# Performance work log

Measured on AMD Instinct MI355X. Metric: run time of the kernel, lower is better.

The kernel has to match this reference:

```python
import jax, jax.numpy as jnp
import numpy as np

N = 65536        # lattice nodes (256x256 grid)
E_RAND = 1_000_000  # non-self-loop causal edges (~16 per node)
T = 65           # max edge type after add_self_loops (type 1 = self loop)
FIN = 8
FOUT = 8
B = 16           # batch of spin configurations


def setup_inputs() -> dict:
    key = jax.random.key(0)
    k1, k2, k3, k4, k5, k6 = jax.random.split(key, 6)
    x = jax.random.normal(k1, (N, FIN, B), dtype=jnp.float32)
    bound = 1.0 / np.sqrt(FIN)  # matches reset_parameters uniform init
    W = jax.random.uniform(k2, (T, FOUT, FIN), jnp.float32, -bound, bound)
    b = jax.random.uniform(k3, (T, FOUT), jnp.float32, -bound, bound)
    # add_self_loops: identity edges with type 1, other types shifted to 2..T
    loops = jnp.arange(N, dtype=jnp.int32)
    src = jnp.concatenate([loops, jax.random.randint(k4, (E_RAND,), 0, N, dtype=jnp.int32)])
    tgt = jnp.concatenate([loops, jax.random.randint(k5, (E_RAND,), 0, N, dtype=jnp.int32)])
    etype = jnp.concatenate([
        jnp.ones((N,), dtype=jnp.int32),
        jax.random.randint(k6, (E_RAND,), 2, T + 1, dtype=jnp.int32),
    ])
    return {"x": x, "W": W, "b": b, "src": src, "tgt": tgt, "etype": etype}


def reference(x, W, b, src, tgt, etype):
    # Faithful to GraphConvLayer.forward (depth=None): the expanded sparse
    # weight matrix assigns a unique [FOUT,FIN] block W[t-1] to every base
    # edge (tgt,src) of type t, and torch.sparse.mm sums duplicate entries.
    Wg = W[etype - 1]                              # [E, FOUT, FIN] gather by edge type
    msg = jnp.einsum('eoi,eib->eob', Wg, x[src])   # per-edge messages [E, FOUT, B]
    y = jax.ops.segment_sum(msg, tgt, num_segments=N)       # [N, FOUT, B]
    # bias graph expanded with source_dim=1, multiplied by ones -> per-edge bias
    yb = jax.ops.segment_sum(b[etype - 1], tgt, num_segments=N)  # [N, FOUT]
    return y + yb[:, :, None]
```

## Files before the change

### kernel.cpp

```cpp
#include <hip/hip_runtime.h>


#define CAP 48
#define ROWSTRIDE 52
#define DUMMY_T 65
#define NT 66
#define BUCKETS 512
#define BNODES 128
#define BCAP 2304
#define CHUNK 4096

typedef short bf16x8 __attribute__((ext_vector_type(8)));
typedef float f32x4 __attribute__((ext_vector_type(4)));

__device__ __forceinline__ unsigned f2bf(float f) {
    unsigned u = __float_as_uint(f);
    return (u + 0x7FFFu + ((u >> 16) & 1u)) >> 16;
}

__device__ __forceinline__ int qperm(int r) { return (r == 1) ? 2 : (r == 2) ? 1 : r; }

__global__ __launch_bounds__(256)
void bin_a(const float* __restrict__ x, const float* __restrict__ W,
           const int* __restrict__ rsrc, const int* __restrict__ rtgt,
           const int* __restrict__ rety,
           int* __restrict__ gcnt, unsigned* __restrict__ bdata,
           uint4* __restrict__ xt, uint4* __restrict__ Wbf, int N, int ER, int nchunk) {
    __shared__ int hist[BUCKETS];
    __shared__ int curs[BUCKETS];
    __shared__ int gbase[BUCKETS];
    int bid = blockIdx.x, tid = threadIdx.x;

    if (bid < nchunk) {
        hist[tid] = 0; hist[tid + 256] = 0;
        curs[tid] = 0; curs[tid + 256] = 0;
        __syncthreads();
        int e0 = bid * CHUNK;
        int lim = ER - e0; if (lim > CHUNK) lim = CHUNK;
        for (int r = tid * 4; r < lim; r += 1024) {
            if (r + 4 <= lim) {
                int4 tv = *reinterpret_cast<const int4*>(rtgt + e0 + r);
                atomicAdd(&hist[tv.x >> 7], 1);
                atomicAdd(&hist[tv.y >> 7], 1);
                atomicAdd(&hist[tv.z >> 7], 1);
                atomicAdd(&hist[tv.w >> 7], 1);
            } else {
                for (int q = r; q < lim; ++q) atomicAdd(&hist[rtgt[e0 + q] >> 7], 1);
            }
        }
        __syncthreads();
        int hv = hist[tid];
        gbase[tid] = hv ? atomicAdd(&gcnt[tid], hv) : 0;
        hv = hist[tid + 256];
        gbase[tid + 256] = hv ? atomicAdd(&gcnt[tid + 256], hv) : 0;
        __syncthreads();
        for (int r = tid * 4; r < lim; r += 1024) {
            if (r + 4 <= lim) {
                int4 tv = *reinterpret_cast<const int4*>(rtgt + e0 + r);
                int4 sv = *reinterpret_cast<const int4*>(rsrc + e0 + r);
                int4 qv = *reinterpret_cast<const int4*>(rety + e0 + r);
                int tt[4] = {tv.x, tv.y, tv.z, tv.w};
                int ss[4] = {sv.x, sv.y, sv.z, sv.w};
                int qq[4] = {qv.x, qv.y, qv.z, qv.w};
#pragma unroll
                for (int u = 0; u < 4; ++u) {
                    int bb = tt[u] >> 7;
                    unsigned pay = (unsigned)(tt[u] & 127) | ((unsigned)ss[u] << 7)
                                 | ((unsigned)(qq[u] - 1) << 23);
                    int pos = gbase[bb] + atomicAdd(&curs[bb], 1);
                    if (pos < BCAP) bdata[(size_t)bb * BCAP + pos] = pay;
                }
            } else {
                for (int q = r; q < lim; ++q) {
                    int e = e0 + q;
                    int t = rtgt[e];
                    int bb = t >> 7;
                    unsigned pay = (unsigned)(t & 127) | ((unsigned)rsrc[e] << 7)
                                 | ((unsigned)(rety[e] - 1) << 23);
                    int pos = gbase[bb] + atomicAdd(&curs[bb], 1);
                    if (pos < BCAP) bdata[(size_t)bb * BCAP + pos] = pay;
                }
            }
        }
    } else if (bid < nchunk + (N * 16) / 256) {
        int p = (bid - nchunk) * 256 + tid;
        int n = p >> 4, j = p & 15;
        const float* xp = x + (size_t)n * 128 + j;
        unsigned w[4];
#pragma unroll
        for (int i = 0; i < 4; ++i)
            w[i] = f2bf(xp[(2 * i) * 16]) | (f2bf(xp[(2 * i + 1) * 16]) << 16);
        xt[p] = make_uint4(w[0], w[1], w[2], w[3]);
    } else {
        for (int i = tid; i < NT * 8; i += 256) {
            uint4 wv = make_uint4(0, 0, 0, 0);
            if (i < 65 * 8) {
                const float* wr = W + (size_t)i * 8;
                wv = make_uint4(f2bf(wr[0]) | (f2bf(wr[1]) << 16),
                                f2bf(wr[2]) | (f2bf(wr[3]) << 16),
                                f2bf(wr[4]) | (f2bf(wr[5]) << 16),
                                f2bf(wr[6]) | (f2bf(wr[7]) << 16));
            }
            Wbf[i] = wv;
        }
    }
}

__global__ __launch_bounds__(256)
void build_b(const int* __restrict__ gcnt, const unsigned* __restrict__ bdata,
             const float* __restrict__ bias, int* __restrict__ nitq,
             float* __restrict__ ybias, unsigned* __restrict__ adj) {
    __shared__ unsigned ladj[BNODES * ROWSTRIDE];
    __shared__ int ldeg[BNODES];
    __shared__ float blds[NT * 8];
    int b = blockIdx.x, tid = threadIdx.x;

    if (tid < BNODES) ldeg[tid] = 0;
    const unsigned DUM = (unsigned)DUMMY_T << 16;
    uint4* l4 = reinterpret_cast<uint4*>(ladj);
#pragma unroll 2
    for (int i = tid; i < BNODES * ROWSTRIDE / 4; i += 256)
        l4[i] = make_uint4(DUM, DUM, DUM, DUM);
    for (int i = tid; i < NT * 8; i += 256)
        blds[i] = (i < 65 * 8) ? bias[i] : 0.f;
    __syncthreads();

    int cnt = gcnt[b]; if (cnt > BCAP) cnt = BCAP;
    const unsigned* bp = bdata + (size_t)b * BCAP;
    for (int i = tid; i < cnt; i += 256) {
        unsigned p = bp[i];
        int tl = (int)(p & 127u);
        int pos = atomicAdd(&ldeg[tl], 1);
        if (pos < CAP)
            ladj[tl * ROWSTRIDE + (pos & ~3) + qperm(pos & 3)] =
                ((p >> 7) & 0xFFFFu) | ((p >> 23) << 16);
    }
    __syncthreads();

    if (tid < BNODES) {
        int node = b * BNODES + tid;
        int d = ldeg[tid]; if (d > CAP) d = CAP;
        ladj[tid * ROWSTRIDE + (d & ~3) + qperm(d & 3)] = (unsigned)node;
        int nq = (d + 4) >> 2;
        nitq[node] = nq;

        float yb[8] = {0.f, 0.f, 0.f, 0.f, 0.f, 0.f, 0.f, 0.f};
        for (int k = 0; k < nq * 4; ++k) {
            unsigned t = ladj[tid * ROWSTRIDE + k] >> 16;
            const float* br = blds + t * 8;
#pragma unroll
            for (int o = 0; o < 8; ++o) yb[o] += br[o];
        }
        float4* yb4 = reinterpret_cast<float4*>(ybias + (size_t)node * 8);
        yb4[0] = make_float4(yb[0], yb[1], yb[2], yb[3]);
        yb4[1] = make_float4(yb[4], yb[5], yb[6], yb[7]);
    }

    __syncthreads();
    const uint4* ls = reinterpret_cast<const uint4*>(ladj);
    uint4* gd = reinterpret_cast<uint4*>(adj + (size_t)b * BNODES * ROWSTRIDE);
#pragma unroll 2
    for (int i = tid; i < BNODES * ROWSTRIDE / 4; i += 256) gd[i] = ls[i];
}

__global__ __launch_bounds__(256)
void gather_mfma(const uint4* __restrict__ xt, const uint4* __restrict__ Wbf,
                 const float4* __restrict__ ybias4, const int* __restrict__ nitq,
                 const unsigned* __restrict__ adjp, float* __restrict__ out, int N) {
    int lane = threadIdx.x & 63;
    int nA = blockIdx.x * 8 + (threadIdx.x >> 6) * 2;
    int nB = nA + 1;
    int j = lane & 15;
    int h = lane >> 4;
    bool aact = ((h & 1) == 0) ? (j < 8) : (j >= 8);
    int rowoff = (h & 1) * 4;

    int nit = max(nitq[nA], nitq[nB]);
    const unsigned* apA = adjp + (size_t)nA * ROWSTRIDE + h;
    const unsigned* apB = adjp + (size_t)nB * ROWSTRIDE + h;

    f32x4 accA = {0.f, 0.f, 0.f, 0.f};
    f32x4 accB = {0.f, 0.f, 0.f, 0.f};

    unsigned pkA = apA[0], pkB = apB[0];
    uint4 xvA = xt[(pkA & 0xFFFFu) * 16 + j];
    uint4 xvB = xt[(pkB & 0xFFFFu) * 16 + j];
    uint4 wvA = Wbf[(aact ? (pkA >> 16) : (unsigned)DUMMY_T) * 8 + (j & 7)];
    uint4 wvB = Wbf[(aact ? (pkB >> 16) : (unsigned)DUMMY_T) * 8 + (j & 7)];

    for (int i = 1; i < nit; ++i) {
        unsigned pkA2 = apA[i * 4], pkB2 = apB[i * 4];
        uint4 xvA2 = xt[(pkA2 & 0xFFFFu) * 16 + j];
        uint4 xvB2 = xt[(pkB2 & 0xFFFFu) * 16 + j];
        uint4 wvA2 = Wbf[(aact ? (pkA2 >> 16) : (unsigned)DUMMY_T) * 8 + (j & 7)];
        uint4 wvB2 = Wbf[(aact ? (pkB2 >> 16) : (unsigned)DUMMY_T) * 8 + (j & 7)];
        accA = __builtin_amdgcn_mfma_f32_16x16x32_bf16(
                   __builtin_bit_cast(bf16x8, wvA), __builtin_bit_cast(bf16x8, xvA), accA, 0, 0, 0);
        accB = __builtin_amdgcn_mfma_f32_16x16x32_bf16(
                   __builtin_bit_cast(bf16x8, wvB), __builtin_bit_cast(bf16x8, xvB), accB, 0, 0, 0);
        xvA = xvA2; wvA = wvA2; xvB = xvB2; wvB = wvB2;
    }
    accA = __builtin_amdgcn_mfma_f32_16x16x32_bf16(
               __builtin_bit_cast(bf16x8, wvA), __builtin_bit_cast(bf16x8, xvA), accA, 0, 0, 0);
    accB = __builtin_amdgcn_mfma_f32_16x16x32_bf16(
               __builtin_bit_cast(bf16x8, wvB), __builtin_bit_cast(bf16x8, xvB), accB, 0, 0, 0);

#pragma unroll
    for (int q = 0; q < 4; ++q) {
        accA[q] += __shfl_xor(accA[q], 32);
        accB[q] += __shfl_xor(accB[q], 32);
    }

    if (lane < 32) {
        float4 ybA = ybias4[nA * 2 + (h & 1)];
        float4 ybB = ybias4[nB * 2 + (h & 1)];
        float* opA = out + (size_t)nA * 128 + rowoff * 16 + j;
        float* opB = out + (size_t)nB * 128 + rowoff * 16 + j;
        opA[0]  = accA[0] + ybA.x;
        opA[16] = accA[1] + ybA.y;
        opA[32] = accA[2] + ybA.z;
        opA[48] = accA[3] + ybA.w;
        opB[0]  = accB[0] + ybB.x;
        opB[16] = accB[1] + ybB.y;
        opB[32] = accB[2] + ybB.z;
        opB[48] = accB[3] + ybB.w;
    }
}

extern "C" void kernel_launch(void* const* d_in, const int* in_sizes, int n_in,
                              void* d_out, int out_size, void* d_ws, size_t ws_size,
                              hipStream_t stream) {
    const float* x     = (const float*)d_in[0];
    const float* W     = (const float*)d_in[1];
    const float* bias  = (const float*)d_in[2];
    const int*   src   = (const int*)d_in[3];
    const int*   tgt   = (const int*)d_in[4];
    const int*   etype = (const int*)d_in[5];
    float*       out   = (float*)d_out;

    const int N  = out_size / 128;
    const int E  = in_sizes[3];
    const int ER = E - N;

    char* ws = (char*)d_ws;
    int*      nitq  = (int*)ws;      ws += (size_t)N * 4;
    unsigned* adj   = (unsigned*)ws; ws += (size_t)N * ROWSTRIDE * 4;
    uint4*    xt    = (uint4*)ws;    ws += (size_t)N * 16 * 16;
    unsigned* bdata = (unsigned*)ws; ws += (size_t)BUCKETS * BCAP * 4;
    float*    ybias = (float*)ws;    ws += (size_t)N * 8 * 4;
    int*      gcnt  = (int*)ws;      ws += (size_t)BUCKETS * 4;
    uint4*    Wbf   = (uint4*)ws;

    hipMemsetAsync(gcnt, 0, (size_t)BUCKETS * 4, stream);
    int nchunk = (ER + CHUNK - 1) / CHUNK;
    bin_a<<<nchunk + (N * 16) / 256 + 1, 256, 0, stream>>>(
        x, W, src + N, tgt + N, etype + N, gcnt, bdata, xt, Wbf, N, ER, nchunk);
    build_b<<<BUCKETS, 256, 0, stream>>>(gcnt, bdata, bias, nitq, ybias, adj);
    gather_mfma<<<N / 8, 256, 0, stream>>>(xt, Wbf, (const float4*)ybias, nitq, adj, out, N);
}
```

Baseline: 77.12 us.

## Fuse adjacency build and MFMA gather into one kernel using shared-memory adjacency

Merges the bucket-to-adjacency build kernel and the MFMA gather kernel into a single 1024-thread kernel per 128-node bucket. The adjacency rows, per-node iteration counts and bias sums stay in shared memory instead of being written to global workspace and read back, which removes one launch and the round trip of roughly 13 MB of adjacency data. In exchange only 512 large blocks run the gather phase, each wave handles 8 nodes serially, and the gather cannot begin until the build phase of its block finishes, which may cut the parallelism available to hide gather latency.

```diff
diff --git a/kernel.cpp b/kernel.cpp
--- a/kernel.cpp
+++ b/kernel.cpp
@@ -106,28 +106,29 @@
     }
 }
 
-__global__ __launch_bounds__(256)
-void build_b(const int* __restrict__ gcnt, const unsigned* __restrict__ bdata,
-             const float* __restrict__ bias, int* __restrict__ nitq,
-             float* __restrict__ ybias, unsigned* __restrict__ adj) {
+__global__ __launch_bounds__(1024, 8)
+void build_gather(const int* __restrict__ gcnt, const unsigned* __restrict__ bdata,
+                  const float* __restrict__ bias, const uint4* __restrict__ xt,
+                  const uint4* __restrict__ Wbf, float* __restrict__ out) {
     __shared__ unsigned ladj[BNODES * ROWSTRIDE];
     __shared__ int ldeg[BNODES];
+    __shared__ int lnit[BNODES];
     __shared__ float blds[NT * 8];
+    __shared__ float lyb[BNODES * 8];
     int b = blockIdx.x, tid = threadIdx.x;
 
     if (tid < BNODES) ldeg[tid] = 0;
     const unsigned DUM = (unsigned)DUMMY_T << 16;
     uint4* l4 = reinterpret_cast<uint4*>(ladj);
 #pragma unroll 2
-    for (int i = tid; i < BNODES * ROWSTRIDE / 4; i += 256)
+    for (int i = tid; i < BNODES * ROWSTRIDE / 4; i += 1024)
         l4[i] = make_uint4(DUM, DUM, DUM, DUM);
-    for (int i = tid; i < NT * 8; i += 256)
-        blds[i] = (i < 65 * 8) ? bias[i] : 0.f;
+    if (tid < NT * 8) blds[tid] = (tid < 65 * 8) ? bias[tid] : 0.f;
     __syncthreads();
 
     int cnt = gcnt[b]; if (cnt > BCAP) cnt = BCAP;
     const unsigned* bp = bdata + (size_t)b * BCAP;
-    for (int i = tid; i < cnt; i += 256) {
+    for (int i = tid; i < cnt; i += 1024) {
         unsigned p = bp[i];
         int tl = (int)(p & 127u);
         int pos = atomicAdd(&ldeg[tl], 1);
@@ -142,7 +143,7 @@
         int d = ldeg[tid]; if (d > CAP) d = CAP;
         ladj[tid * ROWSTRIDE + (d & ~3) + qperm(d & 3)] = (unsigned)node;
         int nq = (d + 4) >> 2;
-        nitq[node] = nq;
+        lnit[tid] = nq;
 
         float yb[8] = {0.f, 0.f, 0.f, 0.f, 0.f, 0.f, 0.f, 0.f};
         for (int k = 0; k < nq * 4; ++k) {
@@ -151,79 +152,73 @@
 #pragma unroll
             for (int o = 0; o < 8; ++o) yb[o] += br[o];
         }
-        float4* yb4 = reinterpret_cast<float4*>(ybias + (size_t)node * 8);
-        yb4[0] = make_float4(yb[0], yb[1], yb[2], yb[3]);
-        yb4[1] = make_float4(yb[4], yb[5], yb[6], yb[7]);
-    }
-
+#pragma unroll
+        for (int o = 0; o < 8; ++o) lyb[tid * 8 + o] = yb[o];
+    }
     __syncthreads();
-    const uint4* ls = reinterpret_cast<const uint4*>(ladj);
-    uint4* gd = reinterpret_cast<uint4*>(adj + (size_t)b * BNODES * ROWSTRIDE);
-#pragma unroll 2
-    for (int i = tid; i < BNODES * ROWSTRIDE / 4; i += 256) gd[i] = ls[i];
-}
-
-__global__ __launch_bounds__(256)
-void gather_mfma(const uint4* __restrict__ xt, const uint4* __restrict__ Wbf,
-                 const float4* __restrict__ ybias4, const int* __restrict__ nitq,
-                 const unsigned* __restrict__ adjp, float* __restrict__ out, int N) {
-    int lane = threadIdx.x & 63;
-    int nA = blockIdx.x * 8 + (threadIdx.x >> 6) * 2;
-    int nB = nA + 1;
+
+    int lane = tid & 63;
+    int wave = tid >> 6;
     int j = lane & 15;
     int h = lane >> 4;
     bool aact = ((h & 1) == 0) ? (j < 8) : (j >= 8);
     int rowoff = (h & 1) * 4;
-
-    int nit = max(nitq[nA], nitq[nB]);
-    const unsigned* apA = adjp + (size_t)nA * ROWSTRIDE + h;
-    const unsigned* apB = adjp + (size_t)nB * ROWSTRIDE + h;
-
-    f32x4 accA = {0.f, 0.f, 0.f, 0.f};
-    f32x4 accB = {0.f, 0.f, 0.f, 0.f};
-
-    unsigned pkA = apA[0], pkB = apB[0];
-    uint4 xvA = xt[(pkA & 0xFFFFu) * 16 + j];
-    uint4 xvB = xt[(pkB & 0xFFFFu) * 16 + j];
-    uint4 wvA = Wbf[(aact ? (pkA >> 16) : (unsigned)DUMMY_T) * 8 + (j & 7)];
-    uint4 wvB = Wbf[(aact ? (pkB >> 16) : (unsigned)DUMMY_T) * 8 + (j & 7)];
-
-    for (int i = 1; i < nit; ++i) {
-        unsigned pkA2 = apA[i * 4], pkB2 = apB[i * 4];
-        uint4 xvA2 = xt[(pkA2 & 0xFFFFu) * 16 + j];
-        uint4 xvB2 = xt[(pkB2 & 0xFFFFu) * 16 + j];
-        uint4 wvA2 = Wbf[(aact ? (pkA2 >> 16) : (unsigned)DUMMY_T) * 8 + (j & 7)];
-        uint4 wvB2 = Wbf[(aact ? (pkB2 >> 16) : (unsigned)DUMMY_T) * 8 + (j & 7)];
+    const float4* ybp = reinterpret_cast<const float4*>(lyb);
+
+    for (int pp = 0; pp < 4; ++pp) {
+        int nAl = (wave << 3) + (pp << 1);
+        int nBl = nAl + 1;
+        int nit = max(lnit[nAl], lnit[nBl]);
+        const unsigned* apA = ladj + nAl * ROWSTRIDE + h;
+        const unsigned* apB = ladj + nBl * ROWSTRIDE + h;
+
+        f32x4 accA = {0.f, 0.f, 0.f, 0.f};
+        f32x4 accB = {0.f, 0.f, 0.f, 0.f};
+
+        unsigned pkA = apA[0], pkB = apB[0];
+        uint4 xvA = xt[(pkA & 0xFFFFu) * 16 + j];
+        uint4 xvB = xt[(pkB & 0xFFFFu) * 16 + j];
+        uint4 wvA = Wbf[(aact ? (pkA >> 16) : (unsigned)DUMMY_T) * 8 + (j & 7)];
+        uint4 wvB = Wbf[(aact ? (pkB >> 16) : (unsigned)DUMMY_T) * 8 + (j & 7)];
+
+        for (int i = 1; i < nit; ++i) {
+            unsigned pkA2 = apA[i * 4], pkB2 = apB[i * 4];
+            uint4 xvA2 = xt[(pkA2 & 0xFFFFu) * 16 + j];
+            uint4 xvB2 = xt[(pkB2 & 0xFFFFu) * 16 + j];
+            uint4 wvA2 = Wbf[(aact ? (pkA2 >> 16) : (unsigned)DUMMY_T) * 8 + (j & 7)];
+            uint4 wvB2 = Wbf[(aact ? (pkB2 >> 16) : (unsigned)DUMMY_T) * 8 + (j & 7)];
+            accA = __builtin_amdgcn_mfma_f32_16x16x32_bf16(
+                       __builtin_bit_cast(bf16x8, wvA), __builtin_bit_cast(bf16x8, xvA), accA, 0, 0, 0);
+            accB = __builtin_amdgcn_mfma_f32_16x16x32_bf16(
+                       __builtin_bit_cast(bf16x8, wvB), __builtin_bit_cast(bf16x8, xvB), accB, 0, 0, 0);
+            xvA = xvA2; wvA = wvA2; xvB = xvB2; wvB = wvB2;
+        }
         accA = __builtin_amdgcn_mfma_f32_16x16x32_bf16(
                    __builtin_bit_cast(bf16x8, wvA), __builtin_bit_cast(bf16x8, xvA), accA, 0, 0, 0);
         accB = __builtin_amdgcn_mfma_f32_16x16x32_bf16(
                    __builtin_bit_cast(bf16x8, wvB), __builtin_bit_cast(bf16x8, xvB), accB, 0, 0, 0);
-        xvA = xvA2; wvA = wvA2; xvB = xvB2; wvB = wvB2;
-    }
-    accA = __builtin_amdgcn_mfma_f32_16x16x32_bf16(
-               __builtin_bit_cast(bf16x8, wvA), __builtin_bit_cast(bf16x8, xvA), accA, 0, 0, 0);
-    accB = __builtin_amdgcn_mfma_f32_16x16x32_bf16(
-               __builtin_bit_cast(bf16x8, wvB), __builtin_bit_cast(bf16x8, xvB), accB, 0, 0, 0);
-
-#pragma unroll
-    for (int q = 0; q < 4; ++q) {
-        accA[q] += __shfl_xor(accA[q], 32);
-        accB[q] += __shfl_xor(accB[q], 32);
-    }
-
-    if (lane < 32) {
-        float4 ybA = ybias4[nA * 2 + (h & 1)];
-        float4 ybB = ybias4[nB * 2 + (h & 1)];
-        float* opA = out + (size_t)nA * 128 + rowoff * 16 + j;
-        float* opB = out + (size_t)nB * 128 + rowoff * 16 + j;
-        opA[0]  = accA[0] + ybA.x;
-        opA[16] = accA[1] + ybA.y;
-        opA[32] = accA[2] + ybA.z;
-        opA[48] = accA[3] + ybA.w;
-        opB[0]  = accB[0] + ybB.x;
-        opB[16] = accB[1] + ybB.y;
-        opB[32] = accB[2] + ybB.z;
-        opB[48] = accB[3] + ybB.w;
+
+#pragma unroll
+        for (int q = 0; q < 4; ++q) {
+            accA[q] += __shfl_xor(accA[q], 32);
+            accB[q] += __shfl_xor(accB[q], 32);
+        }
+
+        if (lane < 32) {
+            float4 ybA = ybp[nAl * 2 + (h & 1)];
+            float4 ybB = ybp[nBl * 2 + (h & 1)];
+            size_t nA = (size_t)b * BNODES + nAl;
+            float* opA = out + nA * 128 + rowoff * 16 + j;
+            float* opB = opA + 128;
+            opA[0]  = accA[0] + ybA.x;
+            opA[16] = accA[1] + ybA.y;
+            opA[32] = accA[2] + ybA.z;
+            opA[48] = accA[3] + ybA.w;
+            opB[0]  = accB[0] + ybB.x;
+            opB[16] = accB[1] + ybB.y;
+            opB[32] = accB[2] + ybB.z;
+            opB[48] = accB[3] + ybB.w;
+        }
     }
 }
 
@@ -243,11 +238,8 @@
     const int ER = E - N;
 
     char* ws = (char*)d_ws;
-    int*      nitq  = (int*)ws;      ws += (size_t)N * 4;
-    unsigned* adj   = (unsigned*)ws; ws += (size_t)N * ROWSTRIDE * 4;
     uint4*    xt    = (uint4*)ws;    ws += (size_t)N * 16 * 16;
     unsigned* bdata = (unsigned*)ws; ws += (size_t)BUCKETS * BCAP * 4;
-    float*    ybias = (float*)ws;    ws += (size_t)N * 8 * 4;
     int*      gcnt  = (int*)ws;      ws += (size_t)BUCKETS * 4;
     uint4*    Wbf   = (uint4*)ws;
 
@@ -255,6 +247,5 @@
     int nchunk = (ER + CHUNK - 1) / CHUNK;
     bin_a<<<nchunk + (N * 16) / 256 + 1, 256, 0, stream>>>(
         x, W, src + N, tgt + N, etype + N, gcnt, bdata, xt, Wbf, N, ER, nchunk);
-    build_b<<<BUCKETS, 256, 0, stream>>>(gcnt, bdata, bias, nitq, ybias, adj);
-    gather_mfma<<<N / 8, 256, 0, stream>>>(xt, Wbf, (const float4*)ybias, nitq, adj, out, N);
-}
+    build_gather<<<BUCKETS, 1024, 0, stream>>>(gcnt, bdata, bias, xt, Wbf, out);
+}
```

Measured after the change: 72.65 us. 1.06x faster.
